# Optimization experiments

Measured on AMD Instinct MI355X. Metric: run time of the kernel, lower is better.

Reference implementation:

```python
import jax, jax.numpy as jnp
import numpy as np
from jax import lax

G = 64; ELL = 0.18; VOX = ELL / G
C_VIEWS = 6; H_IMG = 256; W_IMG = 256
MAX_N = 2048; PT = 0.25; MT = 0.25; FILL = 0.45
CHUNK = 256; RADIUS_CLIP = 2.0; NEAR = 0.01


def _rotz(a):
    c, s = jnp.cos(a), jnp.sin(a)
    z = jnp.zeros_like(c); o = jnp.ones_like(c)
    return jnp.stack([jnp.stack([c, -s, z]), jnp.stack([s, c, z]), jnp.stack([z, z, o])])


def _quat_to_mat4(q):
    # faithful replication of quaternion_matrix_torch_batch (incl. its asymmetries), fp32
    eps = 4 * np.finfo(np.float32).eps
    n = jnp.sum(q * q, 1)
    qs = q * jnp.sqrt(2.0 / jnp.where(n < eps, 1.0, n))[:, None]
    o = jnp.einsum('bi,bj->bij', qs, qs)
    one = jnp.ones_like(n); zero = jnp.zeros_like(n)
    row0 = jnp.stack([1.0 - o[:, 2, 2] - o[:, 3, 3], o[:, 1, 2] - o[:, 3, 0], o[:, 1, 3] + o[:, 2, 0], zero], 1)
    row1 = jnp.stack([o[:, 1, 2] - o[:, 3, 0], one, o[:, 2, 3] - o[:, 1, 0], zero], 1)
    row2 = jnp.stack([o[:, 1, 3] - o[:, 2, 0], o[:, 2, 3] + o[:, 1, 0], 1.0 - o[:, 1, 1] - o[:, 2, 2], zero], 1)
    row3 = jnp.stack([zero, zero, zero, one], 1)
    M = jnp.stack([row0, row1, row2, row3], 1)
    return jnp.where((n < eps)[:, None, None], jnp.eye(4, dtype=q.dtype), M)


def _quat_from_mat4(m):
    m00, m01, m02 = m[:, 0, 0], m[:, 0, 1], m[:, 0, 2]
    m10, m11, m12 = m[:, 1, 0], m[:, 1, 1], m[:, 1, 2]
    m20, m21, m22 = m[:, 2, 0], m[:, 2, 1], m[:, 2, 2]
    r0 = jnp.stack([m00 - m11 - m22, m01 + m10, m02 + m20, m21 - m12], 1)
    r1 = jnp.stack([m01 + m10, m11 - m00 - m22, m12 + m21, m02 - m20], 1)
    r2 = jnp.stack([m02 + m20, m12 + m21, m22 - m00 - m11, m10 - m01], 1)
    r3 = jnp.stack([m21 - m12, m02 - m20, m10 - m01, m00 + m11 + m22], 1)
    K = jnp.stack([r0, r1, r2, r3], 1) / 3.0
    _, V = jnp.linalg.eigh(K)
    q = V[:, :, -1][:, jnp.array([3, 0, 1, 2])]
    return jnp.where(q[:, :1] < 0.0, -q, q)


def _splat(means, quats, scales, opac, colors, viewmat, K, bg):
    R3, t3 = viewmat[:3, :3], viewmat[:3, 3]
    cam = means @ R3.T + t3
    x, y, z = cam[:, 0], cam[:, 1], cam[:, 2]
    fx, fy, cx, cy = K[0, 0], K[1, 1], K[0, 2], K[1, 2]
    qn = quats / (jnp.linalg.norm(quats, axis=1, keepdims=True) + 1e-12)
    w, qx, qy, qz = qn[:, 0], qn[:, 1], qn[:, 2], qn[:, 3]
    Rq = jnp.stack([
        jnp.stack([1 - 2 * (qy * qy + qz * qz), 2 * (qx * qy - w * qz), 2 * (qx * qz + w * qy)], 1),
        jnp.stack([2 * (qx * qy + w * qz), 1 - 2 * (qx * qx + qz * qz), 2 * (qy * qz - w * qx)], 1),
        jnp.stack([2 * (qx * qz - w * qy), 2 * (qy * qz + w * qx), 1 - 2 * (qx * qx + qy * qy)], 1)], 1)
    cov3 = jnp.einsum('nij,nj,nkj->nik', Rq, scales ** 2, Rq)
    covc = jnp.einsum('ij,njk,lk->nil', R3, cov3, R3)
    rz = 1.0 / z
    zn = jnp.zeros_like(z)
    J = jnp.stack([jnp.stack([fx * rz, zn, -fx * x * rz * rz], 1),
                   jnp.stack([zn, fy * rz, -fy * y * rz * rz], 1)], 1)  # [N,2,3]
    cov2 = jnp.einsum('nij,njk,nlk->nil', J, covc, J)
    a2 = cov2[:, 0, 0] + 0.3; b2 = cov2[:, 0, 1]; c2 = cov2[:, 1, 1] + 0.3  # gsplat screen dilation
    det = a2 * c2 - b2 * b2
    det_s = jnp.where(det > 1e-12, det, 1.0)
    ca = c2 / det_s; cb = -b2 / det_s; cc = a2 / det_s  # conic
    lam = 0.5 * (a2 + c2) + jnp.sqrt(jnp.maximum(0.25 * (a2 - c2) ** 2 + b2 * b2, 1e-12))
    radius = jnp.ceil(3.0 * jnp.sqrt(lam))
    mu_x = fx * x * rz + cx; mu_y = fy * y * rz + cy
    valid = (z > NEAR) & (det > 1e-12) & (radius > RADIUS_CLIP)
    op = jnp.where(valid, opac, 0.0)
    order = jnp.argsort(z)  # front-to-back
    gac = lambda a: a[order].reshape(-1, CHUNK, *a.shape[1:])
    chunks = (gac(mu_x), gac(mu_y), gac(ca), gac(cb), gac(cc), gac(op), gac(colors))
    xs = jnp.arange(W_IMG, dtype=means.dtype) + 0.5
    ys = jnp.arange(H_IMG, dtype=means.dtype) + 0.5

    @jax.checkpoint
    def body(carry, ch):
        rgb, T = carry
        ux, uy, A, B, Cc, o_, col = ch
        dx = xs[None, None, :] - ux[:, None, None]          # [c,1,W]->[c,H,W]
        dy = ys[None, :, None] - uy[:, None, None]
        sigma = 0.5 * (A[:, None, None] * dx * dx + Cc[:, None, None] * dy * dy) + B[:, None, None] * dx * dy
        alpha = o_[:, None, None] * jnp.exp(-sigma)
        alpha = jnp.where((sigma >= 0) & (alpha >= 1.0 / 255.0), jnp.minimum(alpha, 0.999), 0.0)
        cp = jnp.cumprod(1.0 - alpha, axis=0)
        Tin = jnp.concatenate([jnp.ones_like(cp[:1]), cp[:-1]], 0)  # exclusive transmittance in chunk
        wgt = alpha * Tin * T[None]
        rgb = rgb + jnp.einsum('nhw,nc->hwc', wgt, col)
        return (rgb, T * cp[-1]), None

    init = (jnp.zeros((H_IMG, W_IMG, 3), means.dtype), jnp.ones((H_IMG, W_IMG), means.dtype))
    (rgb, T), _ = lax.scan(body, init, chunks)
    alpha_img = 1.0 - T
    rgb = jnp.clip(rgb + T[..., None] * bg, 0.0, 1.0)
    return rgb[None], alpha_img[None, :, :, None]


def _forward(mask, img, p_3d, angle, grid, Ks, viewmats, w1, b1, w2, b2, scale_param, background, view_num):
    m = mask[0]; im = img[0]
    Rz = _rotz(angle)
    # ---- shape carving: project canonical grid into all views ----
    pw = grid @ Rz.T + p_3d                                   # [V,3]
    cam = jnp.einsum('cij,vj->cvi', viewmats[:, :3, :3], pw) + viewmats[:, None, :3, 3]
    z = cam[..., 2]
    proj = jnp.einsum('cij,cvj->cvi', Ks, cam)
    u = proj[..., 0] / z; v = proj[..., 1] / z
    ui = jnp.clip(jnp.round(u).astype(jnp.int32), 0, W_IMG - 1)
    vi = jnp.clip(jnp.round(v).astype(jnp.int32), 0, H_IMG - 1)
    inb = (u >= 0) & (u < W_IMG) & (v >= 0) & (v < H_IMG) & (z > NEAR)
    cidx = jnp.arange(C_VIEWS)[:, None]
    inside = inb & (m[cidx, vi, ui] > 0.5)
    csamp = im[cidx, vi, ui]                                  # [C,V,3]
    wv = inside.astype(grid.dtype)
    frac = wv.mean(0)
    col = (wv[..., None] * csamp).sum(0) / jnp.maximum(wv.sum(0), 1.0)[:, None]
    col = jnp.where((frac >= 1.0 - 1e-6)[:, None], col, FILL)
    volume = jnp.concatenate([10.0 * frac[None] - 5.0, col.T,
                              jnp.zeros((4, grid.shape[0]), grid.dtype)], 0)  # [8, G^3] (ablation pad)
    # ---- gaussian param extraction (static top-k instead of threshold search) ----
    probs = jax.nn.sigmoid(volume[0] - MT)
    _, idx = lax.top_k(probs, MAX_N)
    feats = volume[:, idx].T                                  # [N,8]
    h = jax.nn.relu(feats @ w1 + b1)
    out = h @ w2 + b2
    quats, scl, _op, cols, dmu = jnp.split(out, [4, 7, 8, 11], axis=1)
    colors = jnp.clip(jax.nn.sigmoid(cols), 0.0, 0.99)
    scales = jnp.exp(scl + scale_param[0])
    opac = jax.nn.sigmoid(jnp.clip((probs[idx] - PT) / (1.0 - PT), 0.0, 1.0))
    means = grid[idx] + 2.0 * VOX * jnp.tanh(dmu)
    # ---- pose transform ----
    means = means @ Rz.T + p_3d
    Rz4 = jnp.eye(4, dtype=means.dtype).at[:3, :3].set(Rz)
    r = jnp.einsum('ij,bjk->bik', Rz4, _quat_to_mat4(quats))
    quats = _quat_from_mat4(r)
    return _splat(means, quats, scales, opac, colors, viewmats[view_num], Ks[view_num], background)


def setup_inputs() -> dict:
    key = jax.random.key(0)
    ks = jax.random.split(key, 6)
    mask = jax.random.uniform(ks[0], (1, C_VIEWS, H_IMG, W_IMG), jnp.float32)
    img = jax.random.uniform(ks[1], (1, C_VIEWS, H_IMG, W_IMG, 3), jnp.float32)
    p_3d = jax.random.normal(ks[2], (3,), jnp.float32) * 0.02
    angle = jax.random.uniform(ks[3], (), jnp.float32) * 2.0 * np.pi
    lin = np.linspace(-ELL / 2, ELL / 2, G, dtype=np.float32)
    gx, gy, gz = np.meshgrid(lin, lin, lin, indexing='ij')
    grid = jnp.asarray(np.stack([gx, gy, gz], -1).reshape(-1, 3))
    Kmat = np.array([[300.0, 0.0, W_IMG / 2], [0.0, 300.0, H_IMG / 2], [0.0, 0.0, 1.0]], np.float32)
    Ks = jnp.asarray(np.stack([Kmat] * C_VIEWS))
    vms = []
    up = np.array([0.0, 0.0, 1.0])
    for i in range(C_VIEWS):
        th = 2 * np.pi * i / C_VIEWS
        eye = np.array([0.8 * np.cos(th), 0.8 * np.sin(th), 0.25])
        f = -eye / np.linalg.norm(eye)
        r = np.cross(f, up); r = r / np.linalg.norm(r)
        d = np.cross(f, r)
        vm = np.eye(4, dtype=np.float32)
        vm[:3, :3] = np.stack([r, d, f]).astype(np.float32)
        vm[:3, 3] = -vm[:3, :3] @ eye.astype(np.float32)
        vms.append(vm)
    viewmats = jnp.asarray(np.stack(vms))
    w1 = jax.random.normal(ks[4], (8, 128), jnp.float32) * 0.3
    b1 = jnp.zeros((128,), jnp.float32)
    w2 = jax.random.normal(ks[5], (128, 14), jnp.float32) * 0.2
    b2 = jnp.zeros((14,), jnp.float32)
    scale_param = jnp.full((1,), -5.5, jnp.float32)
    background = jnp.ones((3,), jnp.float32)
    return dict(mask=mask, img=img, p_3d=p_3d, angle=angle, grid=grid, Ks=Ks, viewmats=viewmats,
                w1=w1, b1=b1, w2=w2, b2=b2, scale_param=scale_param, background=background, view_num=0)


def reference(mask, img, p_3d, angle, grid, Ks, viewmats, w1, b1, w2, b2, scale_param, background, view_num):
    return _forward(mask, img, p_3d, angle, grid, Ks, viewmats, w1, b1, w2, b2, scale_param, background, view_num)
```

## Files before the change

kernel.cpp:

```cpp
#include <hip/hip_runtime.h>
#include <hip/hip_bf16.h>

namespace {
constexpr int GN   = 262144;
constexpr int CV   = 6;
constexpr int HI   = 256, WI = 256;
constexpr int MAXN = 2048;
constexpr int NBLK = GN / 256;
constexpr int NSEG = 8;
constexpr float NEARZ = 0.01f;
constexpr float FILLC = 0.45f;

constexpr size_t OFF_CNT   = 0;
constexpr size_t OFF_BC    = OFF_CNT + GN;
constexpr size_t OFF_BO    = OFF_BC + 7*NBLK*4;
constexpr size_t OFF_TOT   = OFF_BO + 7*NBLK*4;
constexpr size_t OFF_SEL   = OFF_TOT + 64;
constexpr size_t OFF_SCNT  = OFF_SEL + MAXN*4;
constexpr size_t OFF_PAR   = OFF_SCNT + MAXN*4;
constexpr size_t OFF_KEY   = OFF_PAR + MAXN*12*4;
constexpr size_t OFF_RNK   = OFF_KEY + MAXN*8;
constexpr size_t OFF_SPAR  = OFF_RNK + 8*MAXN*4;
constexpr size_t OFF_PART  = OFF_SPAR + MAXN*12*4;
constexpr size_t WS_NEED   = OFF_PART + (size_t)256*NSEG*256*16;
}

__device__ __forceinline__ float sigm_(float x){ return 1.0f/(1.0f+expf(-x)); }

__global__ void k_count(const float* __restrict__ mask, const float* __restrict__ grid,
                        const float* __restrict__ p3d, const float* __restrict__ angle,
                        const float* __restrict__ Ks, const float* __restrict__ vms,
                        unsigned char* __restrict__ cnt8, int* __restrict__ bc)
{
  int p = blockIdx.x*256 + threadIdx.x;
  float a = angle[0];
  float ca = cosf(a), sa = sinf(a);
  float gx = grid[p*3+0], gy = grid[p*3+1], gz = grid[p*3+2];
  float pwx = ca*gx - sa*gy + p3d[0];
  float pwy = sa*gx + ca*gy + p3d[1];
  float pwz = gz + p3d[2];
  int count = 0;
  for (int c = 0; c < CV; ++c){
    const float* R = vms + c*16;
    float cxx = R[0]*pwx + R[1]*pwy + R[2]*pwz + R[3];
    float cyy = R[4]*pwx + R[5]*pwy + R[6]*pwz + R[7];
    float czz = R[8]*pwx + R[9]*pwy + R[10]*pwz + R[11];
    const float* K = Ks + c*9;
    float u = (K[0]*cxx + K[1]*cyy + K[2]*czz)/czz;
    float v = (K[3]*cxx + K[4]*cyy + K[5]*czz)/czz;
    bool inb = (u>=0.f)&&(u<(float)WI)&&(v>=0.f)&&(v<(float)HI)&&(czz>NEARZ);
    int ui = (int)fminf(fmaxf(rintf(u),0.f),(float)(WI-1));
    int vi = (int)fminf(fmaxf(rintf(v),0.f),(float)(HI-1));
    bool inside = inb && (mask[(c*HI+vi)*WI+ui] > 0.5f);
    count += inside ? 1 : 0;
  }
  cnt8[p] = (unsigned char)count;
  __shared__ int lh[7];
  if (threadIdx.x < 7) lh[threadIdx.x] = 0;
  __syncthreads();
  atomicAdd(&lh[6-count], 1);
  __syncthreads();
  if (threadIdx.x < 7) bc[threadIdx.x*NBLK + blockIdx.x] = lh[threadIdx.x];
}

__global__ void __launch_bounds__(1024) k_scan(const int* __restrict__ bc,
                                               int* __restrict__ bo, int* __restrict__ tot)
{
  int L = blockIdx.x;
  __shared__ int s[NBLK];
  int t = threadIdx.x;
  int v = bc[L*NBLK + t];
  s[t] = v;
  __syncthreads();
  for (int ofs = 1; ofs < NBLK; ofs <<= 1){
    int x = (t >= ofs) ? s[t-ofs] : 0;
    __syncthreads();
    s[t] += x;
    __syncthreads();
  }
  bo[L*NBLK + t] = s[t] - v;
  if (t == NBLK-1) tot[L] = s[NBLK-1];
}

__global__ void k_select(const unsigned char* __restrict__ cnt8,
                         const int* __restrict__ bo, const int* __restrict__ tot,
                         int* __restrict__ sel, int* __restrict__ scnt)
{
  int t = threadIdx.x, blk = blockIdx.x;
  int p = blk*256 + t;
  int cnt = cnt8[p];
  int L = 6 - cnt;
  int lsL = 0;
  #pragma unroll
  for (int l = 0; l < 6; ++l) if (l < L) lsL += tot[l];
  unsigned long long msk[7];
  #pragma unroll
  for (int lv = 0; lv < 7; ++lv) msk[lv] = __ballot(L == lv);
  int lane = t & 63, wv = t >> 6;
  __shared__ int wcnt[4][7];
  if (lane < 7) wcnt[wv][lane] = (int)__popcll(msk[lane]);
  __syncthreads();
  int local = (int)__popcll(msk[L] & ((1ull<<lane)-1ull));
  for (int w = 0; w < wv; ++w) local += wcnt[w][L];
  int pos = lsL + bo[L*NBLK + blk] + local;
  if (pos < MAXN){ sel[pos] = p; scnt[pos] = cnt; }
}

#define JROT(dp,dq,opq, okp1,okq1, okp2,okq2, vp0,vq0,vp1,vq1,vp2,vq2,vp3,vq3)  \
  { float apq_ = opq;                                                           \
    if (fabsf(apq_) > 1e-30f){                                                  \
      float th_ = (dq - dp)/(2.f*apq_);                                         \
      float tt_ = (th_>=0.f?1.f:-1.f)/(fabsf(th_)+sqrtf(th_*th_+1.f));          \
      float c_ = 1.f/sqrtf(tt_*tt_+1.f), s_ = tt_*c_;                           \
      dp -= tt_*apq_; dq += tt_*apq_; opq = 0.f;                                \
      float t1_=okp1, t2_=okq1; okp1 = c_*t1_ - s_*t2_; okq1 = s_*t1_ + c_*t2_; \
      t1_=okp2; t2_=okq2; okp2 = c_*t1_ - s_*t2_; okq2 = s_*t1_ + c_*t2_;       \
      t1_=vp0; t2_=vq0; vp0 = c_*t1_ - s_*t2_; vq0 = s_*t1_ + c_*t2_;           \
      t1_=vp1; t2_=vq1; vp1 = c_*t1_ - s_*t2_; vq1 = s_*t1_ + c_*t2_;           \
      t1_=vp2; t2_=vq2; vp2 = c_*t1_ - s_*t2_; vq2 = s_*t1_ + c_*t2_;           \
      t1_=vp3; t2_=vq3; vp3 = c_*t1_ - s_*t2_; vq3 = s_*t1_ + c_*t2_;           \
    } }

__global__ void __launch_bounds__(256) k_mlp_params(
    const float* __restrict__ mask, const float* __restrict__ img,
    const float* __restrict__ grid, const float* __restrict__ p3d,
    const float* __restrict__ angle, const float* __restrict__ Ks,
    const float* __restrict__ vms, const float* __restrict__ w1,
    const float* __restrict__ b1, const float* __restrict__ w2,
    const float* __restrict__ b2, const float* __restrict__ scp,
    const int* __restrict__ vnp, const int* __restrict__ sel,
    const int* __restrict__ scnt, float* __restrict__ par,
    unsigned long long* __restrict__ keys)
{
  int s = blockIdx.x*256 + threadIdx.x;
  if (s >= MAXN) return;
  int p = sel[s];
  int cnt = scnt[s];
  float a = angle[0];
  float cA = cosf(a), sA = sinf(a);
  float gx = grid[p*3+0], gy = grid[p*3+1], gz = grid[p*3+2];
  float pwx = cA*gx - sA*gy + p3d[0];
  float pwy = sA*gx + cA*gy + p3d[1];
  float pwz = gz + p3d[2];
  float sr = 0.f, sg = 0.f, sb = 0.f;
  #pragma unroll
  for (int c = 0; c < CV; ++c){
    const float* R = vms + c*16;
    float cxx = R[0]*pwx + R[1]*pwy + R[2]*pwz + R[3];
    float cyy = R[4]*pwx + R[5]*pwy + R[6]*pwz + R[7];
    float czz = R[8]*pwx + R[9]*pwy + R[10]*pwz + R[11];
    const float* K = Ks + c*9;
    float u = (K[0]*cxx + K[1]*cyy + K[2]*czz)/czz;
    float v = (K[3]*cxx + K[4]*cyy + K[5]*czz)/czz;
    bool inb = (u>=0.f)&&(u<(float)WI)&&(v>=0.f)&&(v<(float)HI)&&(czz>NEARZ);
    int ui = (int)fminf(fmaxf(rintf(u),0.f),(float)(WI-1));
    int vi = (int)fminf(fmaxf(rintf(v),0.f),(float)(HI-1));
    bool inside = inb && (mask[(c*HI+vi)*WI+ui] > 0.5f);
    if (inside){
      const float* ip = img + ((size_t)(c*HI+vi)*WI+ui)*3;
      sr += ip[0]; sg += ip[1]; sb += ip[2];
    }
  }
  float f0 = 10.f*((float)cnt/6.f) - 5.f;
  float f1, f2, f3;
  if (cnt == 6){ f1 = sr/6.f; f2 = sg/6.f; f3 = sb/6.f; }
  else { f1 = FILLC; f2 = FILLC; f3 = FILLC; }
  float o0=b2[0],o1=b2[1],o2=b2[2],o3=b2[3],o4=b2[4],o5=b2[5],o6=b2[6];
  float o7=b2[7],o8=b2[8],o9=b2[9],o10=b2[10],o11=b2[11],o12=b2[12],o13=b2[13];
  for (int j = 0; j < 128; ++j){
    float hj = b1[j] + f0*w1[0*128+j] + f1*w1[1*128+j] + f2*w1[2*128+j] + f3*w1[3*128+j];
    hj = fmaxf(hj, 0.f);
    const float* w2r = w2 + j*14;
    o0 += hj*w2r[0];  o1 += hj*w2r[1];  o2 += hj*w2r[2];  o3 += hj*w2r[3];
    o4 += hj*w2r[4];  o5 += hj*w2r[5];  o6 += hj*w2r[6];  o7 += hj*w2r[7];
    o8 += hj*w2r[8];  o9 += hj*w2r[9];  o10 += hj*w2r[10]; o11 += hj*w2r[11];
    o12 += hj*w2r[12]; o13 += hj*w2r[13];
  }
  float q0=o0, q1=o1, q2=o2, q3=o3;
  float nq = q0*q0+q1*q1+q2*q2+q3*q3;
  float M00,M01,M02,M10,M11,M12,M20,M21,M22;
  if (nq < 4.76837158e-07f){
    M00=1.f;M01=0.f;M02=0.f;M10=0.f;M11=1.f;M12=0.f;M20=0.f;M21=0.f;M22=1.f;
  } else {
    float s2 = 2.0f/nq;
    float e11=q1*q1*s2, e22=q2*q2*s2, e33=q3*q3*s2;
    float e12=q1*q2*s2, e13=q1*q3*s2, e23=q2*q3*s2;
    float e10=q1*q0*s2, e20=q2*q0*s2, e30=q3*q0*s2;
    M00=1.f-e22-e33; M01=e12-e30; M02=e13+e20;
    M10=e12-e30;     M11=1.f;     M12=e23-e10;
    M20=e13-e20;     M21=e23+e10; M22=1.f-e11-e22;
  }
  float r00 = cA*M00 - sA*M10, r01 = cA*M01 - sA*M11, r02 = cA*M02 - sA*M12;
  float r10 = sA*M00 + cA*M10, r11 = sA*M01 + cA*M11, r12 = sA*M02 + cA*M12;
  float r20 = M20, r21 = M21, r22 = M22;
  float d0=(r00-r11-r22)/3.f, d1=(r11-r00-r22)/3.f, d2=(r22-r00-r11)/3.f, d3=(r00+r11+r22)/3.f;
  float g01=(r01+r10)/3.f, g02=(r02+r20)/3.f, g03=(r21-r12)/3.f;
  float g12=(r12+r21)/3.f, g13=(r02-r20)/3.f, g23=(r10-r01)/3.f;
  float v00=1.f,v01=0.f,v02=0.f,v03=0.f;
  float v10=0.f,v11=1.f,v12=0.f,v13=0.f;
  float v20=0.f,v21=0.f,v22=1.f,v23=0.f;
  float v30=0.f,v31=0.f,v32=0.f,v33=1.f;
  for (int sweep = 0; sweep < 7; ++sweep){
    JROT(d0,d1,g01, g02,g12, g03,g13, v00,v01, v10,v11, v20,v21, v30,v31)
    JROT(d0,d2,g02, g01,g12, g03,g23, v00,v02, v10,v12, v20,v22, v30,v32)
    JROT(d0,d3,g03, g01,g13, g02,g23, v00,v03, v10,v13, v20,v23, v30,v33)
    JROT(d1,d2,g12, g01,g02, g13,g23, v01,v02, v11,v12, v21,v22, v31,v32)
    JROT(d1,d3,g13, g01,g03, g12,g23, v01,v03, v11,v13, v21,v23, v31,v33)
    JROT(d2,d3,g23, g02,g03, g12,g13, v02,v03, v12,v13, v22,v23, v32,v33)
  }
  float bv = d0, qw = v30, qx = v00, qy = v10, qz = v20;
  if (d1 > bv){ bv = d1; qw = v31; qx = v01; qy = v11; qz = v21; }
  if (d2 > bv){ bv = d2; qw = v32; qx = v02; qy = v12; qz = v22; }
  if (d3 > bv){ bv = d3; qw = v33; qx = v03; qy = v13; qz = v23; }
  float qlen = sqrtf(qw*qw+qx*qx+qy*qy+qz*qz) + 1e-12f;
  float w = qw/qlen, x = qx/qlen, y = qy/qlen, z = qz/qlen;
  float Rq00 = 1.f-2.f*(y*y+z*z), Rq01 = 2.f*(x*y - w*z), Rq02 = 2.f*(x*z + w*y);
  float Rq10 = 2.f*(x*y + w*z), Rq11 = 1.f-2.f*(x*x+z*z), Rq12 = 2.f*(y*z - w*x);
  float Rq20 = 2.f*(x*z - w*y), Rq21 = 2.f*(y*z + w*x), Rq22 = 1.f-2.f*(x*x+y*y);
  float spv = scp[0];
  float sc0 = expf(o4+spv), sc1 = expf(o5+spv), sc2 = expf(o6+spv);
  float va = sc0*sc0, vb = sc1*sc1, vc = sc2*sc2;
  float C300 = Rq00*Rq00*va + Rq01*Rq01*vb + Rq02*Rq02*vc;
  float C301 = Rq00*Rq10*va + Rq01*Rq11*vb + Rq02*Rq12*vc;
  float C302 = Rq00*Rq20*va + Rq01*Rq21*vb + Rq02*Rq22*vc;
  float C311 = Rq10*Rq10*va + Rq11*Rq11*vb + Rq12*Rq12*vc;
  float C312 = Rq10*Rq20*va + Rq11*Rq21*vb + Rq12*Rq22*vc;
  float C322 = Rq20*Rq20*va + Rq21*Rq21*vb + Rq22*Rq22*vc;
  const float TWOVOX = (float)(2.0*(0.18/64.0));
  float mlx = gx + TWOVOX*tanhf(o11);
  float mly = gy + TWOVOX*tanhf(o12);
  float mlz = gz + TWOVOX*tanhf(o13);
  float mx = cA*mlx - sA*mly + p3d[0];
  float my = sA*mlx + cA*mly + p3d[1];
  float mz = mlz + p3d[2];
  int vn = vnp[0];
  const float* vm = vms + vn*16;
  const float* Kc = Ks + vn*9;
  float xc = vm[0]*mx + vm[1]*my + vm[2]*mz + vm[3];
  float yc = vm[4]*mx + vm[5]*my + vm[6]*mz + vm[7];
  float zc = vm[8]*mx + vm[9]*my + vm[10]*mz + vm[11];
  float R0=vm[0], R1=vm[1], R2=vm[2], R4=vm[4], R5=vm[5], R6=vm[6], R8=vm[8], R9=vm[9], R10=vm[10];
  float T00 = R0*C300 + R1*C301 + R2*C302;
  float T01 = R0*C301 + R1*C311 + R2*C312;
  float T02 = R0*C302 + R1*C312 + R2*C322;
  float T10 = R4*C300 + R5*C301 + R6*C302;
  float T11 = R4*C301 + R5*C311 + R6*C312;
  float T12 = R4*C302 + R5*C312 + R6*C322;
  float T20 = R8*C300 + R9*C301 + R10*C302;
  float T21 = R8*C301 + R9*C311 + R10*C312;
  float T22 = R8*C302 + R9*C312 + R10*C322;
  float cc00 = T00*R0 + T01*R1 + T02*R2;
  float cc01 = T00*R4 + T01*R5 + T02*R6;
  float cc02 = T00*R8 + T01*R9 + T02*R10;
  float cc11 = T10*R4 + T11*R5 + T12*R6;
  float cc12 = T10*R8 + T11*R9 + T12*R10;
  float cc22 = T20*R8 + T21*R9 + T22*R10;
  float fx = Kc[0], fy = Kc[4], cxk = Kc[2], cyk = Kc[5];
  float rz = 1.f/zc;
  float jx0 = fx*rz, jx2 = -fx*xc*rz*rz;
  float jy1 = fy*rz, jy2 = -fy*yc*rz*rz;
  float c2_00 = jx0*jx0*cc00 + 2.f*jx0*jx2*cc02 + jx2*jx2*cc22;
  float c2_01 = jx0*jy1*cc01 + jx0*jy2*cc02 + jx2*jy1*cc12 + jx2*jy2*cc22;
  float c2_11 = jy1*jy1*cc11 + 2.f*jy1*jy2*cc12 + jy2*jy2*cc22;
  float a2 = c2_00 + 0.3f, b2v = c2_01, c2 = c2_11 + 0.3f;
  float det = a2*c2 - b2v*b2v;
  float dets = (det > 1e-12f) ? det : 1.f;
  float conA = c2/dets, conB = -b2v/dets, conC = a2/dets;
  float lam = 0.5f*(a2+c2) + sqrtf(fmaxf(0.25f*(a2-c2)*(a2-c2) + b2v*b2v, 1e-12f));
  float radius = ceilf(3.f*sqrtf(lam));
  float mux = fx*xc*rz + cxk, muy = fy*yc*rz + cyk;
  bool valid = (zc > NEARZ) && (det > 1e-12f) && (radius > 2.0f);
  float prob = sigm_(10.f*((float)cnt/6.f) - 5.f - 0.25f);
  float t01 = fminf(fmaxf((prob - 0.25f)/0.75f, 0.f), 1.f);
  float opac = sigm_(t01);
  float op = valid ? opac : 0.f;
  float colr = fminf(fmaxf(sigm_(o8), 0.f), 0.99f);
  float colg = fminf(fmaxf(sigm_(o9), 0.f), 0.99f);
  float colb = fminf(fmaxf(sigm_(o10), 0.f), 0.99f);
  float tln = (op > 0.f) ? logf(255.f*op) : 0.f;
  float rxp = sqrtf(fmaxf(2.f*tln*a2, 0.f)) + 1.0f;
  float ryp = sqrtf(fmaxf(2.f*tln*c2, 0.f)) + 1.0f;
  float* pr = par + s*12;
  pr[0]=mux; pr[1]=muy; pr[2]=conA; pr[3]=conB; pr[4]=conC;
  pr[5]=op; pr[6]=colr; pr[7]=colg; pr[8]=colb; pr[9]=zc;
  pr[10] = valid ? rxp : -1e9f;
  pr[11] = valid ? ryp : -1e9f;
  unsigned int zb = __float_as_uint(zc);
  zb = (zb & 0x80000000u) ? ~zb : (zb | 0x80000000u);
  keys[s] = ((unsigned long long)zb << 11) | (unsigned long long)s;
}

__global__ void __launch_bounds__(256) k_rank(const unsigned long long* __restrict__ keys,
                                              int* __restrict__ rnk)
{
  int iblk = blockIdx.x >> 3, jblk = blockIdx.x & 7;
  __shared__ unsigned long long jk[256];
  int t = threadIdx.x;
  jk[t] = keys[jblk*256 + t];
  unsigned long long ki = keys[iblk*256 + t];
  __syncthreads();
  int cnt = 0;
  #pragma unroll 8
  for (int n = 0; n < 256; ++n) cnt += (jk[n] < ki) ? 1 : 0;
  rnk[jblk*MAXN + iblk*256 + t] = cnt;
}

__global__ void __launch_bounds__(256) k_finish(const int* __restrict__ rnk,
                                                const float* __restrict__ par,
                                                float* __restrict__ spar)
{
  int i = blockIdx.x*256 + threadIdx.x;
  int rank = 0;
  #pragma unroll
  for (int jb = 0; jb < 8; ++jb) rank += rnk[jb*MAXN + i];
  const float* src = par + i*12;
  float* dst = spar + rank*12;
  #pragma unroll
  for (int q = 0; q < 12; ++q) dst[q] = src[q];
}

__global__ void __launch_bounds__(256) k_raster_part(const float* __restrict__ spar,
                                                     float4* __restrict__ part)
{
  int raw = blockIdx.x;
  int seg = raw & (NSEG-1);
  int tilep = raw >> 3;
  int tile = (tilep*97 + seg*31) & 255;
  int tx = tile & 15, ty = tile >> 4;
  int lx = threadIdx.x & 15, ly = threadIdx.x >> 4;
  float pxc = tx*16 + lx + 0.5f, pyc = ty*16 + ly + 0.5f;
  float tileX0 = tx*16 + 0.5f, tileX1 = tx*16 + 15.5f;
  float tileY0 = ty*16 + 0.5f, tileY1 = ty*16 + 15.5f;
  __shared__ float lp[256*9];
  __shared__ int wbase[4];
  int lane = threadIdx.x & 63, wv = threadIdx.x >> 6;
  const float* gp = spar + (size_t)(seg*256 + threadIdx.x)*12;
  float mux = gp[0], muy = gp[1], op = gp[5], rx = gp[10], ry = gp[11];
  bool keep = (op > 0.f) &&
              (mux + rx >= tileX0) && (mux - rx <= tileX1) &&
              (muy + ry >= tileY0) && (muy - ry <= tileY1);
  unsigned long long m = __ballot(keep);
  if (lane == 0) wbase[wv] = (int)__popcll(m);
  __syncthreads();
  int base = 0, total = 0;
  #pragma unroll
  for (int w = 0; w < 4; ++w){ if (w < wv) base += wbase[w]; total += wbase[w]; }
  if (keep){
    int pos = base + (int)__popcll(m & ((1ull<<lane)-1ull));
    float* dst = lp + pos*9;
    dst[0]=mux; dst[1]=muy; dst[2]=gp[2]; dst[3]=gp[3]; dst[4]=gp[4];
    dst[5]=op;  dst[6]=gp[6]; dst[7]=gp[7]; dst[8]=gp[8];
  }
  __syncthreads();
  float T = 1.f, rr = 0.f, gg = 0.f, bb = 0.f;
  for (int n = 0; n < total; ++n){
    const float* g = lp + n*9;
    float dx = pxc - g[0], dy = pyc - g[1];
    float sig = 0.5f*(g[2]*dx*dx + g[4]*dy*dy) + g[3]*dx*dy;
    float alpha = g[5]*expf(-sig);
    if (sig >= 0.f && alpha >= 1.0f/255.0f){
      alpha = fminf(alpha, 0.999f);
      float wgt = alpha*T;
      rr += wgt*g[6]; gg += wgt*g[7]; bb += wgt*g[8];
      T *= (1.f - alpha);
    }
  }
  part[(size_t)(tile*NSEG + seg)*256 + threadIdx.x] = make_float4(rr, gg, bb, T);
}

__global__ void __launch_bounds__(256) k_combine(const float4* __restrict__ part,
                                                 const float* __restrict__ bg,
                                                 float* __restrict__ outp)
{
  int tile = blockIdx.x;
  int t = threadIdx.x;
  int tx = tile & 15, ty = tile >> 4;
  int px = tx*16 + (t & 15), py = ty*16 + (t >> 4);
  float rr = 0.f, gg = 0.f, bb = 0.f, T = 1.f;
  #pragma unroll
  for (int seg = 0; seg < NSEG; ++seg){
    float4 v = part[(size_t)(tile*NSEG + seg)*256 + t];
    rr += T*v.x; gg += T*v.y; bb += T*v.z; T *= v.w;
  }
  int pix = py*WI + px;
  outp[pix*3+0] = fminf(fmaxf(rr + T*bg[0], 0.f), 1.f);
  outp[pix*3+1] = fminf(fmaxf(gg + T*bg[1], 0.f), 1.f);
  outp[pix*3+2] = fminf(fmaxf(bb + T*bg[2], 0.f), 1.f);
  outp[HI*WI*3 + pix] = 1.f - T;
}

__global__ void __launch_bounds__(256) k_raster_mono(const float* __restrict__ spar,
                                                     const float* __restrict__ bg,
                                                     float* __restrict__ outp)
{
  int tile = blockIdx.x;
  int tx = tile & 15, ty = tile >> 4;
  int lx = threadIdx.x & 15, ly = threadIdx.x >> 4;
  int px = tx*16 + lx, py = ty*16 + ly;
  float pxc = px + 0.5f, pyc = py + 0.5f;
  float tileX0 = tx*16 + 0.5f, tileX1 = tx*16 + 15.5f;
  float tileY0 = ty*16 + 0.5f, tileY1 = ty*16 + 15.5f;
  float T = 1.f, rr = 0.f, gg = 0.f, bb = 0.f;
  __shared__ float lp[256*9];
  __shared__ int wbase[4];
  int lane = threadIdx.x & 63, wv = threadIdx.x >> 6;
  for (int ch = 0; ch < MAXN; ch += 256){
    const float* gp = spar + (size_t)(ch + threadIdx.x)*12;
    float mux = gp[0], muy = gp[1], op = gp[5], rx = gp[10], ry = gp[11];
    bool keep = (op > 0.f) &&
                (mux + rx >= tileX0) && (mux - rx <= tileX1) &&
                (muy + ry >= tileY0) && (muy - ry <= tileY1);
    unsigned long long m = __ballot(keep);
    int wc = (int)__popcll(m);
    __syncthreads();
    if (lane == 0) wbase[wv] = wc;
    __syncthreads();
    int base = 0, total = 0;
    #pragma unroll
    for (int w = 0; w < 4; ++w){ if (w < wv) base += wbase[w]; total += wbase[w]; }
    if (keep){
      int pos = base + (int)__popcll(m & ((1ull<<lane)-1ull));
      float* dst = lp + pos*9;
      dst[0]=mux; dst[1]=muy; dst[2]=gp[2]; dst[3]=gp[3]; dst[4]=gp[4];
      dst[5]=op;  dst[6]=gp[6]; dst[7]=gp[7]; dst[8]=gp[8];
    }
    __syncthreads();
    for (int n = 0; n < total; ++n){
      const float* g = lp + n*9;
      float dx = pxc - g[0], dy = pyc - g[1];
      float sig = 0.5f*(g[2]*dx*dx + g[4]*dy*dy) + g[3]*dx*dy;
      float alpha = g[5]*expf(-sig);
      if (sig >= 0.f && alpha >= 1.0f/255.0f){
        alpha = fminf(alpha, 0.999f);
        float wgt = alpha*T;
        rr += wgt*g[6]; gg += wgt*g[7]; bb += wgt*g[8];
        T *= (1.f - alpha);
      }
    }
  }
  int pix = py*WI + px;
  outp[pix*3+0] = fminf(fmaxf(rr + T*bg[0], 0.f), 1.f);
  outp[pix*3+1] = fminf(fmaxf(gg + T*bg[1], 0.f), 1.f);
  outp[pix*3+2] = fminf(fmaxf(bb + T*bg[2], 0.f), 1.f);
  outp[HI*WI*3 + pix] = 1.f - T;
}

extern "C" void kernel_launch(void* const* d_in, const int* in_sizes, int n_in,
                              void* d_out, int out_size, void* d_ws, size_t ws_size,
                              hipStream_t stream)
{
  const float* mask  = (const float*)d_in[0];
  const float* img   = (const float*)d_in[1];
  const float* p3d   = (const float*)d_in[2];
  const float* angle = (const float*)d_in[3];
  const float* grid  = (const float*)d_in[4];
  const float* Ks    = (const float*)d_in[5];
  const float* vms   = (const float*)d_in[6];
  const float* w1    = (const float*)d_in[7];
  const float* b1    = (const float*)d_in[8];
  const float* w2    = (const float*)d_in[9];
  const float* b2    = (const float*)d_in[10];
  const float* scp   = (const float*)d_in[11];
  const float* bg    = (const float*)d_in[12];
  const int*   vn    = (const int*)d_in[13];
  float* outp = (float*)d_out;
  char* ws = (char*)d_ws;
  unsigned char* cnt8 = (unsigned char*)(ws + OFF_CNT);
  int* bc    = (int*)(ws + OFF_BC);
  int* bo    = (int*)(ws + OFF_BO);
  int* tot   = (int*)(ws + OFF_TOT);
  int* sel   = (int*)(ws + OFF_SEL);
  int* scnt  = (int*)(ws + OFF_SCNT);
  float* par   = (float*)(ws + OFF_PAR);
  unsigned long long* keys = (unsigned long long*)(ws + OFF_KEY);
  int* rnk   = (int*)(ws + OFF_RNK);
  float* spar  = (float*)(ws + OFF_SPAR);
  float4* part = (float4*)(ws + OFF_PART);

  k_count <<<NBLK, 256, 0, stream>>>(mask, grid, p3d, angle, Ks, vms, cnt8, bc);
  k_scan  <<<7, 1024, 0, stream>>>(bc, bo, tot);
  k_select<<<NBLK, 256, 0, stream>>>(cnt8, bo, tot, sel, scnt);
  k_mlp_params<<<MAXN/256, 256, 0, stream>>>(mask, img, grid, p3d, angle, Ks, vms,
                                             w1, b1, w2, b2, scp, vn, sel, scnt, par, keys);
  k_rank  <<<64, 256, 0, stream>>>(keys, rnk);
  k_finish<<<MAXN/256, 256, 0, stream>>>(rnk, par, spar);
  if (ws_size >= WS_NEED){
    k_raster_part<<<256*NSEG, 256, 0, stream>>>(spar, part);
    k_combine    <<<256, 256, 0, stream>>>(part, bg, outp);
  } else {
    k_raster_mono<<<256, 256, 0, stream>>>(spar, bg, outp);
  }
}
```

Baseline: 173.0 us.

## Stage MLP weights in shared memory and spread k_mlp_params over more blocks

The MLP weights (w1 transposed into float4 rows, w2 padded to 16 columns, and both biases) are now copied into LDS once per block, and the inner loop reads them with vector LDS loads instead of scalar global loads. The launch goes from 8 blocks of 256 threads to 32 blocks of 64 threads, so the 2048 selected points are spread over more compute units. The cost is a per-block weight copy and a barrier, and each block now runs a single wavefront.

```diff
diff --git a/kernel.cpp b/kernel.cpp
--- a/kernel.cpp
+++ b/kernel.cpp
@@ -121,7 +121,7 @@
       t1_=vp3; t2_=vq3; vp3 = c_*t1_ - s_*t2_; vq3 = s_*t1_ + c_*t2_;           \
     } }
 
-__global__ void __launch_bounds__(256) k_mlp_params(
+__global__ void __launch_bounds__(64, 1) k_mlp_params(
     const float* __restrict__ mask, const float* __restrict__ img,
     const float* __restrict__ grid, const float* __restrict__ p3d,
     const float* __restrict__ angle, const float* __restrict__ Ks,
@@ -132,8 +132,26 @@
     const int* __restrict__ scnt, float* __restrict__ par,
     unsigned long long* __restrict__ keys)
 {
-  int s = blockIdx.x*256 + threadIdx.x;
-  if (s >= MAXN) return;
+  __shared__ float4 w1t[128];
+  __shared__ float4 w2t[128*4];
+  __shared__ float  b1s[128];
+  __shared__ float  b2s[16];
+  int t = threadIdx.x;
+  for (int j = t; j < 128; j += 64){
+    w1t[j] = make_float4(w1[j], w1[128+j], w1[256+j], w1[384+j]);
+    b1s[j] = b1[j];
+  }
+  {
+    float* w2f = (float*)w2t;
+    for (int i = t; i < 2048; i += 64){
+      int j = i >> 4, c = i & 15;
+      w2f[i] = (c < 14) ? w2[j*14+c] : 0.f;
+    }
+  }
+  if (t < 14) b2s[t] = b2[t];
+  else if (t < 16) b2s[t] = 0.f;
+  __syncthreads();
+  int s = blockIdx.x*64 + t;
   int p = sel[s];
   int cnt = scnt[s];
   float a = angle[0];
@@ -165,16 +183,18 @@
   float f1, f2, f3;
   if (cnt == 6){ f1 = sr/6.f; f2 = sg/6.f; f3 = sb/6.f; }
   else { f1 = FILLC; f2 = FILLC; f3 = FILLC; }
-  float o0=b2[0],o1=b2[1],o2=b2[2],o3=b2[3],o4=b2[4],o5=b2[5],o6=b2[6];
-  float o7=b2[7],o8=b2[8],o9=b2[9],o10=b2[10],o11=b2[11],o12=b2[12],o13=b2[13];
+  float o0=b2s[0],o1=b2s[1],o2=b2s[2],o3=b2s[3],o4=b2s[4],o5=b2s[5],o6=b2s[6];
+  float o7=b2s[7],o8=b2s[8],o9=b2s[9],o10=b2s[10],o11=b2s[11],o12=b2s[12],o13=b2s[13];
+  #pragma unroll 4
   for (int j = 0; j < 128; ++j){
-    float hj = b1[j] + f0*w1[0*128+j] + f1*w1[1*128+j] + f2*w1[2*128+j] + f3*w1[3*128+j];
+    float4 wv = w1t[j];
+    float hj = b1s[j] + f0*wv.x + f1*wv.y + f2*wv.z + f3*wv.w;
     hj = fmaxf(hj, 0.f);
-    const float* w2r = w2 + j*14;
-    o0 += hj*w2r[0];  o1 += hj*w2r[1];  o2 += hj*w2r[2];  o3 += hj*w2r[3];
-    o4 += hj*w2r[4];  o5 += hj*w2r[5];  o6 += hj*w2r[6];  o7 += hj*w2r[7];
-    o8 += hj*w2r[8];  o9 += hj*w2r[9];  o10 += hj*w2r[10]; o11 += hj*w2r[11];
-    o12 += hj*w2r[12]; o13 += hj*w2r[13];
+    float4 wa = w2t[j*4+0], wb = w2t[j*4+1], wc = w2t[j*4+2], wd = w2t[j*4+3];
+    o0 += hj*wa.x;  o1 += hj*wa.y;  o2 += hj*wa.z;  o3 += hj*wa.w;
+    o4 += hj*wb.x;  o5 += hj*wb.y;  o6 += hj*wb.z;  o7 += hj*wb.w;
+    o8 += hj*wc.x;  o9 += hj*wc.y;  o10 += hj*wc.z; o11 += hj*wc.w;
+    o12 += hj*wd.x; o13 += hj*wd.y;
   }
   float q0=o0, q1=o1, q2=o2, q3=o3;
   float nq = q0*q0+q1*q1+q2*q2+q3*q3;
@@ -480,8 +500,8 @@
   k_count <<<NBLK, 256, 0, stream>>>(mask, grid, p3d, angle, Ks, vms, cnt8, bc);
   k_scan  <<<7, 1024, 0, stream>>>(bc, bo, tot);
   k_select<<<NBLK, 256, 0, stream>>>(cnt8, bo, tot, sel, scnt);
-  k_mlp_params<<<MAXN/256, 256, 0, stream>>>(mask, img, grid, p3d, angle, Ks, vms,
-                                             w1, b1, w2, b2, scp, vn, sel, scnt, par, keys);
+  k_mlp_params<<<MAXN/64, 64, 0, stream>>>(mask, img, grid, p3d, angle, Ks, vms,
+                                           w1, b1, w2, b2, scp, vn, sel, scnt, par, keys);
   k_rank  <<<64, 256, 0, stream>>>(keys, rnk);
   k_finish<<<MAXN/256, 256, 0, stream>>>(rnk, par, spar);
   if (ws_size >= WS_NEED){
```

Result: faster. 168.2 us (-2.7%).
